# Kernel tuning notes

Measured on AMD Instinct MI355X. Metric: run time of the kernel, lower is better.

Reference implementation:

```python
import jax, jax.numpy as jnp
import numpy as np

B, C_IN, C_OUT, H, W = 8, 4, 64, 8, 2048


def setup_inputs() -> dict:
    key = jax.random.key(0)
    ks = jax.random.split(key, 7)
    # torch Conv2d default init: U(-s, s) with s = 1/sqrt(fan_in), fan_in = C_in*1*1
    s = 1.0 / np.sqrt(C_IN)
    u = lambda k, shape: jax.random.uniform(k, shape, jnp.float32, -s, s)
    return {
        "x": jax.random.normal(ks[0], (B, C_IN, H, W), jnp.float32),
        "Wq": u(ks[1], (C_OUT, C_IN)), "bq": u(ks[2], (C_OUT,)),
        "Wk": u(ks[3], (C_OUT, C_IN)), "bk": u(ks[4], (C_OUT,)),
        "Wv": u(ks[5], (C_OUT, C_IN)), "bv": u(ks[6], (C_OUT,)),
        "causal": 1,
    }


def reference(x, Wq, bq, Wk, bk, Wv, bv, causal):
    b, c_in, h, w = x.shape
    # 1x1 conv == per-pixel linear over channel axis
    def proj(Wm, bm):
        y = jnp.einsum('bchw,oc->bohw', x, Wm) + bm[None, :, None, None]
        return y.reshape(b, -1, w)              # [B, C_out*H, W]
    Q = proj(Wq, bq)
    K = proj(Wk, bk)
    V = proj(Wv, bv)
    d = Q.shape[1]
    # scores[b,k,l] = sum_d Q[b,d,k] * K[b,d,l] / sqrt(d)   -> [B, W, W]
    scores = jnp.einsum('bdk,bdl->bkl', Q, K) / (float(d) ** 0.5)
    if causal:
        # faithful to torch: triu zeros lower triangle, then any zero -> -inf
        scores = jnp.triu(scores)
        scores = jnp.where(scores != 0, scores, -jnp.inf)
    attn = jax.nn.softmax(scores, axis=-1)
    # x_out[b,d,k] = sum_l V[b,d,l] * attn[b,k,l]
    x_out = jnp.einsum('bdl,bkl->bdk', V, attn).reshape(b, -1, h, w)
    return x_out, scores  # plot_weight is the pre-softmax (masked) scores
```

## Files before the change

### kernel.cpp

```cpp
#include <hip/hip_runtime.h>
#include <math.h>


#define B_ 8
#define W_ 2048
#define D_ 512
#define SCALE_ 0.04419417382415922f
#define NEG_BIG_ (-3.0e38f)

typedef __attribute__((ext_vector_type(8))) short bf16x8;
typedef __attribute__((ext_vector_type(4))) float f32x4;

__device__ __forceinline__ unsigned short f2bf(float x) {
  unsigned int u = __float_as_uint(x);
  u += 0x7fffu + ((u >> 16) & 1u);
  return (unsigned short)(u >> 16);
}
__device__ __forceinline__ float bf2f(unsigned short h) {
  return __uint_as_float(((unsigned int)h) << 16);
}
__device__ __forceinline__ void split2(float x, unsigned short& hi, unsigned short& lo) {
  hi = f2bf(x);
  lo = f2bf(x - bf2f(hi));
}

__device__ __forceinline__ void gl16(const unsigned short* g, unsigned short* l) {
  __builtin_amdgcn_global_load_lds(
      (__attribute__((address_space(1))) void*)const_cast<unsigned short*>(g),
      (__attribute__((address_space(3))) void*)l, 16, 0, 0);
}

__device__ __forceinline__ int swz(int row, int lq) {
  return row * 32 + ((lq ^ ((row >> 1) & 3)) << 3);
}

__global__ __launch_bounds__(256) void proj_qk(
    const float* __restrict__ x,
    const float* __restrict__ Wq, const float* __restrict__ bq,
    const float* __restrict__ Wk, const float* __restrict__ bk,
    unsigned short* __restrict__ Qhi, unsigned short* __restrict__ Qlo,
    unsigned short* __restrict__ Khi, unsigned short* __restrict__ Klo) {
  int idx = blockIdx.x * 256 + threadIdx.x;
  int d = idx & (D_ - 1);
  int w = (idx >> 9) & (W_ - 1);
  int b = idx >> 20;
  int o = d >> 3, h = d & 7;
  const float* xp = x + (((size_t)b * 4) * 8 + h) * W_ + w;
  float x0 = xp[0], x1 = xp[8 * W_], x2 = xp[16 * W_], x3 = xp[24 * W_];
  const float* wq = Wq + o * 4;
  const float* wk = Wk + o * 4;
  float q = bq[o] + wq[0] * x0 + wq[1] * x1 + wq[2] * x2 + wq[3] * x3;
  float k = bk[o] + wk[0] * x0 + wk[1] * x1 + wk[2] * x2 + wk[3] * x3;
  unsigned short h16, l16;
  split2(q, h16, l16); Qhi[idx] = h16; Qlo[idx] = l16;
  split2(k, h16, l16); Khi[idx] = h16; Klo[idx] = l16;
}

__global__ __launch_bounds__(256) void proj_v(
    const float* __restrict__ x,
    const float* __restrict__ Wv, const float* __restrict__ bv,
    unsigned short* __restrict__ Vhi, unsigned short* __restrict__ Vlo) {
  int idx = blockIdx.x * 256 + threadIdx.x;
  int w = idx & (W_ - 1);
  int rest = idx >> 11;
  int d = rest & (D_ - 1);
  int b = rest >> 9;
  int o = d >> 3, h = d & 7;
  const float* xp = x + (((size_t)b * 4) * 8 + h) * W_ + w;
  float x0 = xp[0], x1 = xp[8 * W_], x2 = xp[16 * W_], x3 = xp[24 * W_];
  const float* wv = Wv + o * 4;
  float v = bv[o] + wv[0] * x0 + wv[1] * x1 + wv[2] * x2 + wv[3] * x3;
  unsigned short h16, l16;
  split2(v, h16, l16); Vhi[idx] = h16; Vlo[idx] = l16;
}

__global__ __launch_bounds__(256) void scores_mfma(
    const unsigned short* __restrict__ Qhi, const unsigned short* __restrict__ Qlo,
    const unsigned short* __restrict__ Khi, const unsigned short* __restrict__ Klo,
    float* __restrict__ S, const int* __restrict__ causal_p) {
  int f = (blockIdx.z * 16 + blockIdx.y) * 16 + blockIdx.x;
  int lf = (f & 7) * 256 + (f >> 3);
  int b = lf >> 8;
  int k0 = ((lf >> 4) & 15) * 128;
  int l0 = (lf & 15) * 128;
  int causal = *causal_p;
  int t = threadIdx.x;
  float* Sb = S + (size_t)b * W_ * W_;

  if (causal && (l0 + 127 < k0)) {
    float4 nb = make_float4(NEG_BIG_, NEG_BIG_, NEG_BIG_, NEG_BIG_);
    int row = t >> 1, c0 = (t & 1) * 64;
#pragma unroll
    for (int j = 0; j < 16; j++)
      *(float4*)&Sb[(size_t)(k0 + row) * W_ + l0 + c0 + j * 4] = nb;
    return;
  }

  __shared__ __align__(16) unsigned short qh_s[128 * 32], ql_s[128 * 32];
  __shared__ __align__(16) unsigned short kh_s[128 * 32], kl_s[128 * 32];

  int wave = t >> 6, lane = t & 63;
  int wk0 = (wave >> 1) * 64, wl0 = (wave & 1) * 64;
  int lr = lane & 15, lq = lane >> 4;

  const unsigned short* Qhb = Qhi + ((size_t)b * W_ + k0) * D_;
  const unsigned short* Qlb = Qlo + ((size_t)b * W_ + k0) * D_;
  const unsigned short* Khb = Khi + ((size_t)b * W_ + l0) * D_;
  const unsigned short* Klb = Klo + ((size_t)b * W_ + l0) * D_;

  int srow0 = t >> 2, sq = t & 3;
  int srow1 = srow0 + 64;
  size_t g0 = (size_t)srow0 * D_ + ((sq ^ ((srow0 >> 1) & 3)) << 3);
  size_t g1 = (size_t)srow1 * D_ + ((sq ^ ((srow1 >> 1) & 3)) << 3);
  int a0 = t * 8, a1 = t * 8 + 2048;

  f32x4 acc[4][4];
#pragma unroll
  for (int i = 0; i < 4; i++)
#pragma unroll
    for (int j = 0; j < 4; j++) acc[i][j] = (f32x4){0.f, 0.f, 0.f, 0.f};

  for (int d0 = 0; d0 < D_; d0 += 32) {
    gl16(Qhb + g0 + d0, &qh_s[a0]);
    gl16(Qhb + g1 + d0, &qh_s[a1]);
    gl16(Qlb + g0 + d0, &ql_s[a0]);
    gl16(Qlb + g1 + d0, &ql_s[a1]);
    gl16(Khb + g0 + d0, &kh_s[a0]);
    gl16(Khb + g1 + d0, &kh_s[a1]);
    gl16(Klb + g0 + d0, &kl_s[a0]);
    gl16(Klb + g1 + d0, &kl_s[a1]);
    __syncthreads();

    bf16x8 ah[4], al[4], bh[4], bl[4];
#pragma unroll
    for (int mt = 0; mt < 4; mt++) {
      int a = swz(wk0 + mt * 16 + lr, lq);
      ah[mt] = *(const bf16x8*)&qh_s[a];
      al[mt] = *(const bf16x8*)&ql_s[a];
    }
#pragma unroll
    for (int nt = 0; nt < 4; nt++) {
      int a = swz(wl0 + nt * 16 + lr, lq);
      bh[nt] = *(const bf16x8*)&kh_s[a];
      bl[nt] = *(const bf16x8*)&kl_s[a];
    }
#pragma unroll
    for (int mt = 0; mt < 4; mt++)
#pragma unroll
      for (int nt = 0; nt < 4; nt++) {
        acc[mt][nt] = __builtin_amdgcn_mfma_f32_16x16x32_bf16(ah[mt], bh[nt], acc[mt][nt], 0, 0, 0);
        acc[mt][nt] = __builtin_amdgcn_mfma_f32_16x16x32_bf16(ah[mt], bl[nt], acc[mt][nt], 0, 0, 0);
        acc[mt][nt] = __builtin_amdgcn_mfma_f32_16x16x32_bf16(al[mt], bh[nt], acc[mt][nt], 0, 0, 0);
      }
    __syncthreads();
  }

#pragma unroll
  for (int mt = 0; mt < 4; mt++)
#pragma unroll
    for (int nt = 0; nt < 4; nt++)
#pragma unroll
      for (int r = 0; r < 4; r++) {
        int k = k0 + wk0 + mt * 16 + lq * 4 + r;
        int l = l0 + wl0 + nt * 16 + lr;
        float s = acc[mt][nt][r] * SCALE_;
        if (causal && (l < k || s == 0.0f)) s = NEG_BIG_;
        Sb[(size_t)k * W_ + l] = s;
      }
}

__global__ __launch_bounds__(256) void softmax_stats_kernel(
    const float* __restrict__ S, float* __restrict__ mrow, float* __restrict__ invrow) {
  int row = blockIdx.x;
  const float* Sr = S + (size_t)row * W_;
  int t = threadIdx.x;
  float v[8];
  *(float4*)&v[0] = *(const float4*)&Sr[t * 8];
  *(float4*)&v[4] = *(const float4*)&Sr[t * 8 + 4];
  float mx = -INFINITY;
#pragma unroll
  for (int r = 0; r < 8; r++) mx = fmaxf(mx, v[r]);
#pragma unroll
  for (int off = 1; off < 64; off <<= 1) mx = fmaxf(mx, __shfl_xor(mx, off, 64));
  __shared__ float redm[4];
  __shared__ float reds[4];
  int wid = t >> 6, lane = t & 63;
  if (lane == 0) redm[wid] = mx;
  __syncthreads();
  mx = fmaxf(fmaxf(redm[0], redm[1]), fmaxf(redm[2], redm[3]));
  float sum = 0.f;
#pragma unroll
  for (int r = 0; r < 8; r++) sum += __expf(v[r] - mx);
#pragma unroll
  for (int off = 1; off < 64; off <<= 1) sum += __shfl_xor(sum, off, 64);
  if (lane == 0) reds[wid] = sum;
  __syncthreads();
  if (t == 0) {
    float s = reds[0] + reds[1] + reds[2] + reds[3];
    mrow[row] = mx;
    invrow[row] = 1.0f / s;
  }
}

__global__ __launch_bounds__(512) void out_fused(
    const unsigned short* __restrict__ Vhi, const unsigned short* __restrict__ Vlo,
    const float* __restrict__ S,
    const float* __restrict__ mrow, const float* __restrict__ invrow,
    float* __restrict__ O, const int* __restrict__ causal_p) {
  int f = blockIdx.z * 32 + blockIdx.x;
  int lf = (f & 7) * 32 + (f >> 3);
  int b = lf >> 5;
  int r5 = lf & 31;
  int k0 = (r5 >> 1) * 128;
  int dh = r5 & 1;
  int causal = *causal_p;
  int t = threadIdx.x;
  int wave = t >> 6, lane = t & 63;
  int wd0 = (wave >> 1) * 64;
  int wk0 = (wave & 1) * 64;
  int lr = lane & 15, lq = lane >> 4;

  __shared__ __align__(16) unsigned short vh_s[2][256 * 32], vl_s[2][256 * 32];
  __shared__ __align__(16) unsigned short ph_s[2][128 * 32], pl_s[2][128 * 32];

  const unsigned short* Vhb = Vhi + ((size_t)b * D_ + dh * 256) * W_;
  const unsigned short* Vlb = Vlo + ((size_t)b * D_ + dh * 256) * W_;
  const float* Sb = S + (size_t)b * W_ * W_;

  int vrow0 = t >> 2, vc = t & 3;
  int vxor = (vc ^ ((vrow0 >> 1) & 3)) << 3;
  const unsigned short* VhA = Vhb + (size_t)vrow0 * W_ + vxor;
  const unsigned short* VhB = VhA + (size_t)128 * W_;
  const unsigned short* VlA = Vlb + (size_t)vrow0 * W_ + vxor;
  const unsigned short* VlB = VlA + (size_t)128 * W_;
  int a0 = t * 8, a1 = t * 8 + 4096;

  int prow = t >> 2, pc = t & 3;
  const float* Srow = Sb + (size_t)(k0 + prow) * W_ + pc * 8;
  int paddr = prow * 32 + ((pc ^ ((prow >> 1) & 3)) << 3);
  float m = mrow[(size_t)b * W_ + k0 + prow];
  float inv = invrow[(size_t)b * W_ + k0 + prow];

  f32x4 acc[4][4];
#pragma unroll
  for (int i = 0; i < 4; i++)
#pragma unroll
    for (int j = 0; j < 4; j++) acc[i][j] = (f32x4){0.f, 0.f, 0.f, 0.f};

  int lstart = causal ? k0 : 0;
  int nch = (W_ - lstart) >> 5;

  float4 s0_, s1_;
  auto stageV = [&](int buf, int l) {
    gl16(VhA + l, &vh_s[buf][a0]);
    gl16(VhB + l, &vh_s[buf][a1]);
    gl16(VlA + l, &vl_s[buf][a0]);
    gl16(VlB + l, &vl_s[buf][a1]);
  };
  auto loadS = [&](int l) {
    s0_ = *(const float4*)&Srow[l];
    s1_ = *(const float4*)&Srow[l + 4];
  };
  auto writeP = [&](int buf) {
    float p[8];
    p[0] = __expf(s0_.x - m) * inv; p[1] = __expf(s0_.y - m) * inv;
    p[2] = __expf(s0_.z - m) * inv; p[3] = __expf(s0_.w - m) * inv;
    p[4] = __expf(s1_.x - m) * inv; p[5] = __expf(s1_.y - m) * inv;
    p[6] = __expf(s1_.z - m) * inv; p[7] = __expf(s1_.w - m) * inv;
    unsigned short hi8[8] __attribute__((aligned(16)));
    unsigned short lo8[8] __attribute__((aligned(16)));
#pragma unroll
    for (int j = 0; j < 8; j++) split2(p[j], hi8[j], lo8[j]);
    *(uint4*)&ph_s[buf][paddr] = *(uint4*)hi8;
    *(uint4*)&pl_s[buf][paddr] = *(uint4*)lo8;
  };

  stageV(0, lstart);
  loadS(lstart);
  writeP(0);
  __syncthreads();

  for (int ci = 0; ci < nch; ci++) {
    int cur = ci & 1, nxt = cur ^ 1;
    bool pre = (ci + 1 < nch);
    if (pre) {
      int ln = lstart + (ci + 1) * 32;
      stageV(nxt, ln);
      loadS(ln);
    }

    bf16x8 ah[4], al[4], bh[4], bl[4];
#pragma unroll
    for (int mt = 0; mt < 4; mt++) {
      int a = swz(wd0 + mt * 16 + lr, lq);
      ah[mt] = *(const bf16x8*)&vh_s[cur][a];
      al[mt] = *(const bf16x8*)&vl_s[cur][a];
    }
#pragma unroll
    for (int nt = 0; nt < 4; nt++) {
      int a = swz(wk0 + nt * 16 + lr, lq);
      bh[nt] = *(const bf16x8*)&ph_s[cur][a];
      bl[nt] = *(const bf16x8*)&pl_s[cur][a];
    }
#pragma unroll
    for (int mt = 0; mt < 4; mt++)
#pragma unroll
      for (int nt = 0; nt < 4; nt++) {
        acc[mt][nt] = __builtin_amdgcn_mfma_f32_16x16x32_bf16(ah[mt], bh[nt], acc[mt][nt], 0, 0, 0);
        acc[mt][nt] = __builtin_amdgcn_mfma_f32_16x16x32_bf16(ah[mt], bl[nt], acc[mt][nt], 0, 0, 0);
        acc[mt][nt] = __builtin_amdgcn_mfma_f32_16x16x32_bf16(al[mt], bh[nt], acc[mt][nt], 0, 0, 0);
      }

    if (pre) writeP(nxt);
    __syncthreads();
  }

#pragma unroll
  for (int mt = 0; mt < 4; mt++)
#pragma unroll
    for (int nt = 0; nt < 4; nt++)
#pragma unroll
      for (int r = 0; r < 4; r++) {
        int d = dh * 256 + wd0 + mt * 16 + lq * 4 + r;
        int k = k0 + wk0 + nt * 16 + lr;
        O[((size_t)b * D_ + d) * W_ + k] = acc[mt][nt][r];
      }
}

extern "C" void kernel_launch(void* const* d_in, const int* in_sizes, int n_in,
                              void* d_out, int out_size, void* d_ws, size_t ws_size,
                              hipStream_t stream) {
  const float* x  = (const float*)d_in[0];
  const float* Wq = (const float*)d_in[1];
  const float* bq = (const float*)d_in[2];
  const float* Wk = (const float*)d_in[3];
  const float* bk = (const float*)d_in[4];
  const float* Wv = (const float*)d_in[5];
  const float* bv = (const float*)d_in[6];
  const int* causal = (const int*)d_in[7];

  float* out = (float*)d_out;
  float* x_out = out;
  float* S = out + (size_t)B_ * D_ * W_;

  const size_t NQ = (size_t)B_ * W_ * D_;
  unsigned short* wsu = (unsigned short*)d_ws;
  unsigned short* Qhi = wsu;
  unsigned short* Qlo = wsu + NQ;
  unsigned short* Khi = wsu + 2 * NQ;
  unsigned short* Klo = wsu + 3 * NQ;
  unsigned short* Vhi = wsu + 4 * NQ;
  unsigned short* Vlo = wsu + 5 * NQ;
  float* mrow   = (float*)(wsu + 6 * NQ);
  float* invrow = mrow + (size_t)B_ * W_;

  int nproj = (int)(NQ / 256);
  proj_qk<<<nproj, 256, 0, stream>>>(x, Wq, bq, Wk, bk, Qhi, Qlo, Khi, Klo);
  proj_v<<<nproj, 256, 0, stream>>>(x, Wv, bv, Vhi, Vlo);
  scores_mfma<<<dim3(W_ / 128, W_ / 128, B_), 256, 0, stream>>>(Qhi, Qlo, Khi, Klo, S, causal);
  softmax_stats_kernel<<<B_ * W_, 256, 0, stream>>>(S, mrow, invrow);
  out_fused<<<dim3(32, 1, B_), 512, 0, stream>>>(Vhi, Vlo, S, mrow, invrow, x_out, causal);
}
```

Before: 434.1 us.

## Unroll output pipeline by two, raise MFMA priority, skip masked reads in softmax stats

The output kernel's double-buffered loop is unrolled by two with fixed buffer indices, and the scores for the next chunk are loaded earlier, so the P-tile writes overlap with the MFMA work. s_setprio raises wave priority around the MFMA blocks in both the scores and output kernels. The softmax stats kernel no longer reads score segments that lie fully below the causal diagonal and fills them with the mask value instead. The aim is to cut global traffic and issue stalls, at the cost of more complex control flow and extra register pressure.

New measurement: 416.9 us. -4.0%, faster.

```diff
diff --git a/kernel.cpp b/kernel.cpp
--- a/kernel.cpp
+++ b/kernel.cpp
@@ -144,6 +144,7 @@
       bh[nt] = *(const bf16x8*)&kh_s[a];
       bl[nt] = *(const bf16x8*)&kl_s[a];
     }
+    __builtin_amdgcn_s_setprio(1);
 #pragma unroll
     for (int mt = 0; mt < 4; mt++)
 #pragma unroll
@@ -152,6 +153,7 @@
         acc[mt][nt] = __builtin_amdgcn_mfma_f32_16x16x32_bf16(ah[mt], bl[nt], acc[mt][nt], 0, 0, 0);
         acc[mt][nt] = __builtin_amdgcn_mfma_f32_16x16x32_bf16(al[mt], bh[nt], acc[mt][nt], 0, 0, 0);
       }
+    __builtin_amdgcn_s_setprio(0);
     __syncthreads();
   }
 
@@ -170,13 +172,21 @@
 }
 
 __global__ __launch_bounds__(256) void softmax_stats_kernel(
-    const float* __restrict__ S, float* __restrict__ mrow, float* __restrict__ invrow) {
+    const float* __restrict__ S, float* __restrict__ mrow, float* __restrict__ invrow,
+    const int* __restrict__ causal_p) {
   int row = blockIdx.x;
+  int k = row & (W_ - 1);
+  int causal = *causal_p;
   const float* Sr = S + (size_t)row * W_;
   int t = threadIdx.x;
   float v[8];
-  *(float4*)&v[0] = *(const float4*)&Sr[t * 8];
-  *(float4*)&v[4] = *(const float4*)&Sr[t * 8 + 4];
+  if (causal && (t * 8 + 8 <= k)) {
+#pragma unroll
+    for (int r = 0; r < 8; r++) v[r] = NEG_BIG_;
+  } else {
+    *(float4*)&v[0] = *(const float4*)&Sr[t * 8];
+    *(float4*)&v[4] = *(const float4*)&Sr[t * 8 + 4];
+  }
   float mx = -INFINITY;
 #pragma unroll
   for (int r = 0; r < 8; r++) mx = fmaxf(mx, v[r]);
@@ -250,58 +260,42 @@
   int lstart = causal ? k0 : 0;
   int nch = (W_ - lstart) >> 5;
 
-  float4 s0_, s1_;
   auto stageV = [&](int buf, int l) {
     gl16(VhA + l, &vh_s[buf][a0]);
     gl16(VhB + l, &vh_s[buf][a1]);
     gl16(VlA + l, &vl_s[buf][a0]);
     gl16(VlB + l, &vl_s[buf][a1]);
   };
-  auto loadS = [&](int l) {
-    s0_ = *(const float4*)&Srow[l];
-    s1_ = *(const float4*)&Srow[l + 4];
-  };
-  auto writeP = [&](int buf) {
+  auto writeP = [&](unsigned short* __restrict__ ph, unsigned short* __restrict__ pl,
+                    float4 s0, float4 s1) {
     float p[8];
-    p[0] = __expf(s0_.x - m) * inv; p[1] = __expf(s0_.y - m) * inv;
-    p[2] = __expf(s0_.z - m) * inv; p[3] = __expf(s0_.w - m) * inv;
-    p[4] = __expf(s1_.x - m) * inv; p[5] = __expf(s1_.y - m) * inv;
-    p[6] = __expf(s1_.z - m) * inv; p[7] = __expf(s1_.w - m) * inv;
+    p[0] = __expf(s0.x - m) * inv; p[1] = __expf(s0.y - m) * inv;
+    p[2] = __expf(s0.z - m) * inv; p[3] = __expf(s0.w - m) * inv;
+    p[4] = __expf(s1.x - m) * inv; p[5] = __expf(s1.y - m) * inv;
+    p[6] = __expf(s1.z - m) * inv; p[7] = __expf(s1.w - m) * inv;
     unsigned short hi8[8] __attribute__((aligned(16)));
     unsigned short lo8[8] __attribute__((aligned(16)));
 #pragma unroll
     for (int j = 0; j < 8; j++) split2(p[j], hi8[j], lo8[j]);
-    *(uint4*)&ph_s[buf][paddr] = *(uint4*)hi8;
-    *(uint4*)&pl_s[buf][paddr] = *(uint4*)lo8;
+    *(uint4*)&ph[paddr] = *(uint4*)hi8;
+    *(uint4*)&pl[paddr] = *(uint4*)lo8;
   };
-
-  stageV(0, lstart);
-  loadS(lstart);
-  writeP(0);
-  __syncthreads();
-
-  for (int ci = 0; ci < nch; ci++) {
-    int cur = ci & 1, nxt = cur ^ 1;
-    bool pre = (ci + 1 < nch);
-    if (pre) {
-      int ln = lstart + (ci + 1) * 32;
-      stageV(nxt, ln);
-      loadS(ln);
-    }
-
+  auto compute = [&](const unsigned short* vh, const unsigned short* vl,
+                     const unsigned short* ph, const unsigned short* pl) {
     bf16x8 ah[4], al[4], bh[4], bl[4];
 #pragma unroll
     for (int mt = 0; mt < 4; mt++) {
       int a = swz(wd0 + mt * 16 + lr, lq);
-      ah[mt] = *(const bf16x8*)&vh_s[cur][a];
-      al[mt] = *(const bf16x8*)&vl_s[cur][a];
+      ah[mt] = *(const bf16x8*)&vh[a];
+      al[mt] = *(const bf16x8*)&vl[a];
     }
 #pragma unroll
     for (int nt = 0; nt < 4; nt++) {
       int a = swz(wk0 + nt * 16 + lr, lq);
-      bh[nt] = *(const bf16x8*)&ph_s[cur][a];
-      bl[nt] = *(const bf16x8*)&pl_s[cur][a];
-    }
+      bh[nt] = *(const bf16x8*)&ph[a];
+      bl[nt] = *(const bf16x8*)&pl[a];
+    }
+    __builtin_amdgcn_s_setprio(1);
 #pragma unroll
     for (int mt = 0; mt < 4; mt++)
 #pragma unroll
@@ -310,8 +304,37 @@
         acc[mt][nt] = __builtin_amdgcn_mfma_f32_16x16x32_bf16(ah[mt], bl[nt], acc[mt][nt], 0, 0, 0);
         acc[mt][nt] = __builtin_amdgcn_mfma_f32_16x16x32_bf16(al[mt], bh[nt], acc[mt][nt], 0, 0, 0);
       }
-
-    if (pre) writeP(nxt);
+    __builtin_amdgcn_s_setprio(0);
+  };
+
+  float4 sE0, sE1, sO0, sO1;
+
+  sE0 = *(const float4*)&Srow[lstart];      sE1 = *(const float4*)&Srow[lstart + 4];
+  sO0 = *(const float4*)&Srow[lstart + 32]; sO1 = *(const float4*)&Srow[lstart + 36];
+  stageV(0, lstart);
+  writeP(&ph_s[0][0], &pl_s[0][0], sE0, sE1);
+  __syncthreads();
+
+  for (int ci = 0; ci < nch; ci += 2) {
+    int base = lstart + ci * 32;
+    if (ci + 2 < nch) {
+      sE0 = *(const float4*)&Srow[base + 64];
+      sE1 = *(const float4*)&Srow[base + 68];
+    }
+    stageV(1, base + 32);
+    writeP(&ph_s[1][0], &pl_s[1][0], sO0, sO1);
+    compute(&vh_s[0][0], &vl_s[0][0], &ph_s[0][0], &pl_s[0][0]);
+    __syncthreads();
+    bool more = (ci + 2 < nch);
+    if (ci + 3 < nch) {
+      sO0 = *(const float4*)&Srow[base + 96];
+      sO1 = *(const float4*)&Srow[base + 100];
+    }
+    if (more) {
+      stageV(0, base + 64);
+      writeP(&ph_s[0][0], &pl_s[0][0], sE0, sE1);
+    }
+    compute(&vh_s[1][0], &vl_s[1][0], &ph_s[1][0], &pl_s[1][0]);
     __syncthreads();
   }
 
@@ -358,6 +381,6 @@
   proj_qk<<<nproj, 256, 0, stream>>>(x, Wq, bq, Wk, bk, Qhi, Qlo, Khi, Klo);
   proj_v<<<nproj, 256, 0, stream>>>(x, Wv, bv, Vhi, Vlo);
   scores_mfma<<<dim3(W_ / 128, W_ / 128, B_), 256, 0, stream>>>(Qhi, Qlo, Khi, Klo, S, causal);
-  softmax_stats_kernel<<<B_ * W_, 256, 0, stream>>>(S, mrow, invrow);
+  softmax_stats_kernel<<<B_ * W_, 256, 0, stream>>>(S, mrow, invrow, causal);
   out_fused<<<dim3(32, 1, B_), 512, 0, stream>>>(Vhi, Vlo, S, mrow, invrow, x_out, causal);
 }
```
